# Performance work log

Measured on AMD Instinct MI355X. Metric: run time of the kernel, lower is better.

The kernel has to match this reference:

```python
import jax, jax.numpy as jnp
import numpy as np


def _masked(scores, mask):
    return jnp.where(mask == 0, -jnp.inf, scores)


def setup_inputs() -> dict:
    key = jax.random.key(0)
    ks = jax.random.split(key, 4)
    B, H, S, D = 2, 12, 4096, 64
    blk = 64
    nb = S // blk          # 64 blocks
    nw = nb - 2            # 62 windows
    R = 3                  # random blocks per window
    return {
        'query': jax.random.normal(ks[0], (B, H, S, D), dtype=jnp.float32),
        'key': jax.random.normal(ks[1], (B, H, S, D), dtype=jnp.float32),
        'value': jax.random.normal(ks[2], (B, H, S, D), dtype=jnp.float32),
        'q_mask': jnp.ones((B, 1, S, 1), dtype=jnp.float32),
        'kv_mask': jnp.ones((B, 1, 1, S), dtype=jnp.float32),
        'band_mask': jnp.ones((B, 1, nb - 4, blk, 3 * blk), dtype=jnp.float32),
        'q_block_mask': jnp.ones((B, nb, blk), dtype=jnp.float32),
        'kv_block_mask': jnp.ones((B, nb, blk), dtype=jnp.float32),
        'random_attn': jax.random.randint(ks[3], (H, nw, R), 0, nb, dtype=jnp.int32),
        'q_block_size': blk,
        'kv_block_size': blk,
    }


def reference(query, key, value, q_mask, kv_mask, band_mask, q_block_mask,
              kv_block_mask, random_attn, q_block_size, kv_block_size):
    B, H, S, D = query.shape
    Skv = key.shape[2]
    qb, kb = q_block_size, kv_block_size
    nb, nkb = S // qb, Skv // kb
    scale = 1.0 / (D ** 0.5)

    # expand random indices over batch: [B,H,nw,R]
    ra = jnp.broadcast_to(random_attn[None].astype(jnp.int32),
                          (B,) + random_attn.shape)
    nw, R = ra.shape[2], ra.shape[3]
    bidx = jnp.arange(B)[:, None, None, None]
    hidx = jnp.arange(H)[None, :, None, None]

    # random mask: [B,H,nw,qb,R*kb]
    rm = kv_block_mask[bidx, ra].reshape(B, H, nw, R * kb)
    random_mask = jnp.einsum('blq,bhlk->bhlqk', q_block_mask[:, 1:-1], rm)

    bq = query.reshape(B, H, nb, qb, D)
    bk = key.reshape(B, H, nkb, kb, D)
    bv = value.reshape(B, H, nkb, kb, D)

    # gathered random blocks: [B,H,nw,R*kb,D]
    sk = bk[bidx, hidx, ra].reshape(B, H, nw, R * kb, D)
    sv = bv[bidx, hidx, ra].reshape(B, H, nw, R * kb, D)

    # --- first query block: attends to everything ---
    p1 = jnp.einsum('bhqd,bhkd->bhqk', bq[:, :, 0], key) * scale
    a1 = jax.nn.softmax(_masked(p1, kv_mask), axis=-1)
    c1 = jnp.einsum('bhqk,bhkd->bhqd', a1, value)[:, :, None]

    # --- second query block ---
    k2 = jnp.concatenate([bk[:, :, 0], bk[:, :, 1], bk[:, :, 2], bk[:, :, -1],
                          sk[:, :, 0]], axis=2)
    v2 = jnp.concatenate([bv[:, :, 0], bv[:, :, 1], bv[:, :, 2], bv[:, :, -1],
                          sv[:, :, 0]], axis=2)
    p2 = jnp.einsum('bhqd,bhkd->bhqk', bq[:, :, 1], k2) * scale
    seq_pad = jnp.concatenate([kv_mask[:, :, :, :3 * kb],
                               kv_mask[:, :, :, -kb:],
                               jnp.ones_like(random_mask[:, :1, 0, :1])], axis=3)
    rand_pad = jnp.concatenate([jnp.ones_like(p2[:, :, :, :4 * kb]),
                                random_mask[:, :, 0]], axis=3)
    a2 = jax.nn.softmax(_masked(p2, jnp.minimum(seq_pad, rand_pad)), axis=-1)
    c2 = jnp.einsum('bhqk,bhkd->bhqd', a2, v2)[:, :, None]

    # --- middle blocks: window + global(first,last) + random ---
    ebk = jnp.concatenate([bk[:, :, 1:-3], bk[:, :, 2:-2], bk[:, :, 3:-1]], axis=3)
    ebv = jnp.concatenate([bv[:, :, 1:-3], bv[:, :, 2:-2], bv[:, :, 3:-1]], axis=3)
    mq = bq[:, :, 2:-2]  # [B,H,nb-4,qb,D]
    inner = _masked(jnp.einsum('bhlqd,bhlkd->bhlqk', mq, ebk) * scale, band_mask)
    randp = _masked(jnp.einsum('bhlqd,bhlkd->bhlqk', mq, sk[:, :, 1:-1]) * scale,
                    random_mask[:, :, 1:-1])
    fop = _masked(jnp.einsum('bhlqd,bhkd->bhlqk', mq, bk[:, :, 0]) * scale,
                  kv_mask[:, :, :, :kb][:, :, :, None, :])
    lop = _masked(jnp.einsum('bhlqd,bhkd->bhlqk', mq, bk[:, :, -1]) * scale,
                  kv_mask[:, :, :, -kb:][:, :, :, None, :])
    band = jnp.concatenate([fop, inner, lop, randp], axis=-1)
    aw = jax.nn.softmax(band, axis=-1)
    cm = jnp.einsum('bhlqk,bhlkd->bhlqd', aw[..., kb:4 * kb], ebv)
    cm += jnp.einsum('bhlqk,bhlkd->bhlqd', aw[..., 4 * kb:-kb], sv[:, :, 1:-1])
    cm += jnp.einsum('bhlqk,bhkd->bhlqd', aw[..., :kb], bv[:, :, 0])
    cm += jnp.einsum('bhlqk,bhkd->bhlqd', aw[..., -kb:], bv[:, :, -1])

    # --- second-to-last query block ---
    k3 = jnp.concatenate([bk[:, :, 0], bk[:, :, -3], bk[:, :, -2], bk[:, :, -1],
                          sk[:, :, -1]], axis=2)
    v3 = jnp.concatenate([bv[:, :, 0], bv[:, :, -3], bv[:, :, -2], bv[:, :, -1],
                          sv[:, :, -1]], axis=2)
    p3 = jnp.einsum('bhqd,bhkd->bhqk', bq[:, :, -2], k3) * scale
    seq_pad3 = jnp.concatenate([kv_mask[:, :, :, :kb],
                                kv_mask[:, :, :, -3 * kb:],
                                jnp.ones_like(random_mask[:, :1, 0, :1])], axis=3)
    rand_pad3 = jnp.concatenate([jnp.ones_like(p3[:, :, :, :4 * kb]),
                                 random_mask[:, :, -1]], axis=3)
    a3 = jax.nn.softmax(_masked(p3, jnp.minimum(seq_pad3, rand_pad3)), axis=-1)
    c3 = jnp.einsum('bhqk,bhkd->bhqd', a3, v3)[:, :, None]

    # --- last query block: attends to everything ---
    p4 = jnp.einsum('bhqd,bhkd->bhqk', bq[:, :, -1], key) * scale
    a4 = jax.nn.softmax(_masked(p4, kv_mask), axis=-1)
    c4 = jnp.einsum('bhqk,bhkd->bhqd', a4, value)[:, :, None]

    ctx = jnp.concatenate([c1, c2, cm, c3, c4], axis=2)
    return ctx.reshape(B, H, S, D) * q_mask
```

## Files before the change

### kernel.cpp

```cpp
#include <hip/hip_runtime.h>
#include <hip/hip_bf16.h>

#define BB 2
#define HH 12
#define SS 4096
#define DD 64
#define NB_ 64
#define NW_ 62
#define RR 3

#define PARTIAL_FLOATS 4160
#define N_HEAVY_UNITS  (BB * HH * 2)
#define N_CHUNKS       8

using short8 = __attribute__((ext_vector_type(8))) short;
using f32x4  = __attribute__((ext_vector_type(4))) float;

__device__ __forceinline__ int swz(int r, int c) {
    return (r << 6) + ((((c >> 3) ^ r) & 7) << 3) + (c & 7);
}

__device__ __forceinline__ short pack_bf16(float f) {
    __bf16 b = (__bf16)f;
    return (short)__builtin_bit_cast(unsigned short, b);
}

__device__ __forceinline__ short8 load_cvt8_scaled(const float* p, float sc) {
    f32x4 a = *(const f32x4*)p;
    f32x4 b = *(const f32x4*)(p + 4);
    short8 r;
#pragma unroll
    for (int i = 0; i < 4; ++i) {
        r[i]     = pack_bf16(a[i] * sc);
        r[i + 4] = pack_bf16(b[i] * sc);
    }
    return r;
}

template<bool SPLIT>
__global__ __launch_bounds__(256)
void bigbird_main(const float* __restrict__ Q, const float* __restrict__ K,
                  const float* __restrict__ V, const float* __restrict__ qmask,
                  const int* __restrict__ ra, float* __restrict__ Out,
                  float* __restrict__ ws)
{
    __shared__ __align__(16) short KB[2][64 * 64];
    __shared__ __align__(16) short VT[2][64 * 64];
    __shared__ __align__(16) short PB[4][16 * 64];

    const int tid  = threadIdx.x;
    const int w    = tid >> 6;
    const int lane = tid & 63;
    const int g    = lane >> 4;
    const int m    = lane & 15;

    const int idx    = blockIdx.x;
    const int NHEAVY = SPLIT ? (N_HEAVY_UNITS * N_CHUNKS) : N_HEAVY_UNITS;

    bool heavy;
    int  b, h, qb, u = 0, chunk = 0, chunk_base = 0, nlist;
    int  slist[8], vlist[8];

    if (idx < NHEAVY) {
        heavy = true;
        if (SPLIT) { u = idx >> 3; chunk = idx & 7; chunk_base = chunk * 8; nlist = 8; }
        else       { u = idx; chunk_base = 0; nlist = NB_; }
        const int bh = u >> 1;
        b = bh / HH; h = bh % HH;
        qb = (u & 1) ? (NB_ - 1) : 0;
    } else {
        heavy = false;
        const int idx2 = idx - NHEAVY;
        const int qidx = idx2 / (BB * HH);
        const int bh   = idx2 % (BB * HH);
        b = bh / HH; h = bh % HH;
        qb = qidx + 1;
        const int* rp = ra + (h * NW_ + (qb - 1)) * RR;
        if (qb == 1) {
            slist[0] = 0; slist[1] = 1; slist[2] = 2; slist[3] = 63;
            slist[4] = rp[0]; slist[5] = rp[1]; slist[6] = rp[2]; nlist = 7;
#pragma unroll
            for (int i = 0; i < 7; ++i) vlist[i] = slist[i];
        } else if (qb == NB_ - 2) {
            slist[0] = 0; slist[1] = 61; slist[2] = 62; slist[3] = 63;
            slist[4] = rp[0]; slist[5] = rp[1]; slist[6] = rp[2]; nlist = 7;
#pragma unroll
            for (int i = 0; i < 7; ++i) vlist[i] = slist[i];
        } else {
            slist[0] = 0; slist[1] = qb - 1; slist[2] = qb; slist[3] = qb + 1;
            slist[4] = 63; slist[5] = rp[0]; slist[6] = rp[1]; slist[7] = rp[2];
            vlist[0] = 0; vlist[1] = qb - 1; vlist[2] = qb; vlist[3] = qb + 1;
            vlist[4] = rp[0]; vlist[5] = rp[1]; vlist[6] = rp[2]; vlist[7] = 63;
            nlist = 8;
        }
    }

    const size_t base = ((size_t)(b * HH + h)) * SS * DD;

    short8 qa[2];
    {
        const float* qp = Q + base + (size_t)(qb * 64 + w * 16 + m) * DD + g * 8;
        qa[0] = load_cvt8_scaled(qp, 0.125f);
        qa[1] = load_cvt8_scaled(qp + 32, 0.125f);
    }

    f32x4 oacc[4];
#pragma unroll
    for (int t = 0; t < 4; ++t) oacc[t] = (f32x4){0.f, 0.f, 0.f, 0.f};
    float lsum[4] = {0.f, 0.f, 0.f, 0.f};

    const int kr = tid >> 2;
    const int kc = (tid & 3) * 16;
    const int vp = tid & 31;
    const int vd = (tid >> 5) * 8;

    f32x4 kreg[4], vreg[4];
    auto load_kv = [&](int i) {
        const int kbs = heavy ? (chunk_base + i) : slist[i];
        const int kbv = heavy ? (chunk_base + i) : vlist[i];
        const float* kp = K + base + (size_t)(kbs * 64 + kr) * DD + kc;
        kreg[0] = *(const f32x4*)(kp);
        kreg[1] = *(const f32x4*)(kp + 4);
        kreg[2] = *(const f32x4*)(kp + 8);
        kreg[3] = *(const f32x4*)(kp + 12);
        const float* vp0 = V + base + (size_t)(kbv * 64 + 2 * vp) * DD + vd;
        vreg[0] = *(const f32x4*)(vp0);
        vreg[1] = *(const f32x4*)(vp0 + 4);
        vreg[2] = *(const f32x4*)(vp0 + DD);
        vreg[3] = *(const f32x4*)(vp0 + DD + 4);
    };

    load_kv(0);
    int cur = 0;

    for (int it = 0; it < nlist; ++it) {
        {
            short8 s0, s1;
#pragma unroll
            for (int i = 0; i < 4; ++i) {
                s0[i] = pack_bf16(kreg[0][i]); s0[i + 4] = pack_bf16(kreg[1][i]);
                s1[i] = pack_bf16(kreg[2][i]); s1[i + 4] = pack_bf16(kreg[3][i]);
            }
            *(short8*)&KB[cur][swz(kr, kc)]     = s0;
            *(short8*)&KB[cur][swz(kr, kc + 8)] = s1;
#pragma unroll
            for (int i = 0; i < 8; ++i) {
                float f0 = (i < 4) ? vreg[0][i] : vreg[1][i - 4];
                float f1 = (i < 4) ? vreg[2][i] : vreg[3][i - 4];
                unsigned int pk = (unsigned int)(unsigned short)pack_bf16(f0) |
                                  ((unsigned int)(unsigned short)pack_bf16(f1) << 16);
                *(unsigned int*)&VT[cur][swz(vd + i, 2 * vp)] = pk;
            }
        }

        __syncthreads();

        if (it + 1 < nlist) load_kv(it + 1);

        f32x4 sacc[4];
#pragma unroll
        for (int t = 0; t < 4; ++t) sacc[t] = (f32x4){0.f, 0.f, 0.f, 0.f};
        __builtin_amdgcn_s_setprio(1);
#pragma unroll
        for (int ks = 0; ks < 2; ++ks) {
#pragma unroll
            for (int t = 0; t < 4; ++t) {
                short8 bk = *(short8*)&KB[cur][swz(t * 16 + m, g * 8 + ks * 32)];
                sacc[t] = __builtin_amdgcn_mfma_f32_16x16x32_bf16(qa[ks], bk, sacc[t], 0, 0, 0);
            }
        }
        __builtin_amdgcn_s_setprio(0);

#pragma unroll
        for (int t = 0; t < 4; ++t) {
#pragma unroll
            for (int j = 0; j < 4; ++j) {
                const float p = __expf(sacc[t][j]);
                lsum[j] += p;
                PB[w][swz(4 * g + j, t * 16 + m)] = pack_bf16(p);
            }
        }

        __builtin_amdgcn_s_setprio(1);
#pragma unroll
        for (int ks = 0; ks < 2; ++ks) {
            short8 pa = *(short8*)&PB[w][swz(m, g * 8 + ks * 32)];
#pragma unroll
            for (int t = 0; t < 4; ++t) {
                short8 bv = *(short8*)&VT[cur][swz(t * 16 + m, g * 8 + ks * 32)];
                oacc[t] = __builtin_amdgcn_mfma_f32_16x16x32_bf16(pa, bv, oacc[t], 0, 0, 0);
            }
        }
        __builtin_amdgcn_s_setprio(0);

        cur ^= 1;
    }

#pragma unroll
    for (int j = 0; j < 4; ++j)
#pragma unroll
        for (int off = 1; off < 16; off <<= 1) lsum[j] += __shfl_xor(lsum[j], off);

    if (SPLIT && heavy) {
        float* pb = ws + (size_t)(u * N_CHUNKS + chunk) * PARTIAL_FLOATS;
#pragma unroll
        for (int j = 0; j < 4; ++j) {
            const int row = w * 16 + 4 * g + j;
#pragma unroll
            for (int t = 0; t < 4; ++t) pb[row * 64 + t * 16 + m] = oacc[t][j];
            if (m == 0) pb[4096 + row] = lsum[j];
        }
    } else {
#pragma unroll
        for (int j = 0; j < 4; ++j) {
            const int row = qb * 64 + w * 16 + 4 * g + j;
            const float sc = qmask[b * SS + row] / lsum[j];
            float* op = Out + base + (size_t)row * DD + m;
#pragma unroll
            for (int t = 0; t < 4; ++t) op[t * 16] = oacc[t][j] * sc;
        }
    }
}

__global__ __launch_bounds__(256)
void bigbird_combine(const float* __restrict__ ws, const float* __restrict__ qmask,
                     float* __restrict__ Out)
{
    const int u  = blockIdx.x;
    const int bh = u >> 1;
    const int b  = bh / HH;
    const int h  = bh % HH;
    const int qb = (u & 1) ? (NB_ - 1) : 0;

    const int tid = threadIdx.x;
    const int r   = tid >> 2;
    const int s   = tid & 3;

    const float* pb0 = ws + (size_t)u * N_CHUNKS * PARTIAL_FLOATS;

    float L = 0.f;
    f32x4 o0 = {0,0,0,0}, o1 = {0,0,0,0}, o2 = {0,0,0,0}, o3 = {0,0,0,0};
#pragma unroll
    for (int c = 0; c < N_CHUNKS; ++c) {
        const float* pb = pb0 + c * PARTIAL_FLOATS;
        L += pb[4096 + r];
        const float* orow = pb + r * 64 + s * 16;
        f32x4 a0 = *(const f32x4*)(orow);
        f32x4 a1 = *(const f32x4*)(orow + 4);
        f32x4 a2 = *(const f32x4*)(orow + 8);
        f32x4 a3 = *(const f32x4*)(orow + 12);
#pragma unroll
        for (int i = 0; i < 4; ++i) {
            o0[i] += a0[i]; o1[i] += a1[i];
            o2[i] += a2[i]; o3[i] += a3[i];
        }
    }

    const int row = qb * 64 + r;
    const float scme = qmask[b * SS + row] / L;
    float* op = Out + ((size_t)(b * HH + h)) * SS * DD + (size_t)row * DD + s * 16;
#pragma unroll
    for (int i = 0; i < 4; ++i) { o0[i] *= scme; o1[i] *= scme; o2[i] *= scme; o3[i] *= scme; }
    *(f32x4*)(op)      = o0;
    *(f32x4*)(op + 4)  = o1;
    *(f32x4*)(op + 8)  = o2;
    *(f32x4*)(op + 12) = o3;
}

extern "C" void kernel_launch(void* const* d_in, const int* in_sizes, int n_in,
                              void* d_out, int out_size, void* d_ws, size_t ws_size,
                              hipStream_t stream) {
    const float* Q     = (const float*)d_in[0];
    const float* K     = (const float*)d_in[1];
    const float* V     = (const float*)d_in[2];
    const float* qmask = (const float*)d_in[3];
    const int*   ra    = (const int*)d_in[8];
    float* Out = (float*)d_out;
    float* ws  = (float*)d_ws;

    const size_t need = (size_t)N_HEAVY_UNITS * N_CHUNKS * PARTIAL_FLOATS * sizeof(float);
    if (ws_size >= need) {
        const int grid = N_HEAVY_UNITS * N_CHUNKS + BB * HH * (NB_ - 2);
        bigbird_main<true><<<grid, 256, 0, stream>>>(Q, K, V, qmask, ra, Out, ws);
        bigbird_combine<<<N_HEAVY_UNITS, 256, 0, stream>>>((const float*)ws, qmask, Out);
    } else {
        const int grid = N_HEAVY_UNITS + BB * HH * (NB_ - 2);
        bigbird_main<false><<<grid, 256, 0, stream>>>(Q, K, V, qmask, ra, Out, ws);
    }
}
```

Before: 65.50 us.

## Pre-convert K/V to swizzled bf16 tile images and stream via LDS DMA

```diff
diff --git a/kernel.cpp b/kernel.cpp
--- a/kernel.cpp
+++ b/kernel.cpp
@@ -12,6 +12,8 @@
 #define PARTIAL_FLOATS 4160
 #define N_HEAVY_UNITS  (BB * HH * 2)
 #define N_CHUNKS       8
+#define N_TILES        (BB * HH * NB_)
+#define TILE_ELEMS     4096
 
 using short8 = __attribute__((ext_vector_type(8))) short;
 using f32x4  = __attribute__((ext_vector_type(4))) float;
@@ -37,12 +39,221 @@
     return r;
 }
 
+__device__ __forceinline__ void dma16(const short* gsrc, short* lds) {
+    __builtin_amdgcn_global_load_lds(
+        (const __attribute__((address_space(1))) void*)gsrc,
+        (__attribute__((address_space(3))) void*)lds, 16, 0, 0);
+}
+
+__global__ __launch_bounds__(256)
+void bigbird_prepass(const float* __restrict__ K, const float* __restrict__ V,
+                     short* __restrict__ Kimg, short* __restrict__ Vimg)
+{
+    const int tile = blockIdx.x;
+    const int tid  = threadIdx.x;
+    const size_t gbase = (size_t)tile * TILE_ELEMS;
+
+    {
+        const int kr = tid >> 2, kc = (tid & 3) * 16;
+        const float* kp = K + gbase + kr * 64 + kc;
+        f32x4 a0 = *(const f32x4*)(kp);
+        f32x4 a1 = *(const f32x4*)(kp + 4);
+        f32x4 a2 = *(const f32x4*)(kp + 8);
+        f32x4 a3 = *(const f32x4*)(kp + 12);
+        short8 s0, s1;
+#pragma unroll
+        for (int i = 0; i < 4; ++i) {
+            s0[i] = pack_bf16(a0[i]); s0[i + 4] = pack_bf16(a1[i]);
+            s1[i] = pack_bf16(a2[i]); s1[i + 4] = pack_bf16(a3[i]);
+        }
+        short* kt = Kimg + gbase;
+        *(short8*)&kt[swz(kr, kc)]     = s0;
+        *(short8*)&kt[swz(kr, kc + 8)] = s1;
+    }
+    {
+        const int vp = tid & 31, vd = (tid >> 5) * 8;
+        const float* v0 = V + gbase + (2 * vp) * 64 + vd;
+        f32x4 b0 = *(const f32x4*)(v0);
+        f32x4 b1 = *(const f32x4*)(v0 + 4);
+        f32x4 c0 = *(const f32x4*)(v0 + 64);
+        f32x4 c1 = *(const f32x4*)(v0 + 64 + 4);
+        short* vt = Vimg + gbase;
+#pragma unroll
+        for (int i = 0; i < 8; ++i) {
+            float f0 = (i < 4) ? b0[i] : b1[i - 4];
+            float f1 = (i < 4) ? c0[i] : c1[i - 4];
+            unsigned int pk = (unsigned int)(unsigned short)pack_bf16(f0) |
+                              ((unsigned int)(unsigned short)pack_bf16(f1) << 16);
+            *(unsigned int*)&vt[swz(vd + i, 2 * vp)] = pk;
+        }
+    }
+}
+
+__global__ __launch_bounds__(256, 4)
+void bigbird_main_img(const short* __restrict__ Kimg, const short* __restrict__ Vimg,
+                      const float* __restrict__ Q, const float* __restrict__ qmask,
+                      const int* __restrict__ ra, float* __restrict__ Out,
+                      float* __restrict__ part)
+{
+    __shared__ __align__(16) short KB[2][TILE_ELEMS];
+    __shared__ __align__(16) short VT[2][TILE_ELEMS];
+    __shared__ __align__(16) short PB[4][16 * 64];
+
+    const int tid  = threadIdx.x;
+    const int w    = tid >> 6;
+    const int lane = tid & 63;
+    const int g    = lane >> 4;
+    const int m    = lane & 15;
+
+    const int idx    = blockIdx.x;
+    const int NHEAVY = N_HEAVY_UNITS * N_CHUNKS;
+
+    bool heavy;
+    int  b, h, qb, u = 0, chunk_base = 0, chunk = 0, nlist;
+    int  slist[8], vlist[8];
+
+    if (idx < NHEAVY) {
+        heavy = true;
+        u = idx >> 3; chunk = idx & 7; chunk_base = chunk * 8; nlist = 8;
+        const int bh = u >> 1;
+        b = bh / HH; h = bh % HH;
+        qb = (u & 1) ? (NB_ - 1) : 0;
+    } else {
+        heavy = false;
+        const int idx2 = idx - NHEAVY;
+        const int qidx = idx2 / (BB * HH);
+        const int bh   = idx2 % (BB * HH);
+        b = bh / HH; h = bh % HH;
+        qb = qidx + 1;
+        const int* rp = ra + (h * NW_ + (qb - 1)) * RR;
+        if (qb == 1) {
+            slist[0] = 0; slist[1] = 1; slist[2] = 2; slist[3] = 63;
+            slist[4] = rp[0]; slist[5] = rp[1]; slist[6] = rp[2]; nlist = 7;
+#pragma unroll
+            for (int i = 0; i < 7; ++i) vlist[i] = slist[i];
+        } else if (qb == NB_ - 2) {
+            slist[0] = 0; slist[1] = 61; slist[2] = 62; slist[3] = 63;
+            slist[4] = rp[0]; slist[5] = rp[1]; slist[6] = rp[2]; nlist = 7;
+#pragma unroll
+            for (int i = 0; i < 7; ++i) vlist[i] = slist[i];
+        } else {
+            slist[0] = 0; slist[1] = qb - 1; slist[2] = qb; slist[3] = qb + 1;
+            slist[4] = 63; slist[5] = rp[0]; slist[6] = rp[1]; slist[7] = rp[2];
+            vlist[0] = 0; vlist[1] = qb - 1; vlist[2] = qb; vlist[3] = qb + 1;
+            vlist[4] = rp[0]; vlist[5] = rp[1]; vlist[6] = rp[2]; vlist[7] = 63;
+            nlist = 8;
+        }
+    }
+
+    const int    bh_lin = b * HH + h;
+    const size_t base   = (size_t)bh_lin * SS * DD;
+    const short* Kbh    = Kimg + (size_t)bh_lin * NB_ * TILE_ELEMS;
+    const short* Vbh    = Vimg + (size_t)bh_lin * NB_ * TILE_ELEMS;
+
+    short8 qa[2];
+    {
+        const float* qp = Q + base + (size_t)(qb * 64 + w * 16 + m) * DD + g * 8;
+        qa[0] = load_cvt8_scaled(qp, 0.125f);
+        qa[1] = load_cvt8_scaled(qp + 32, 0.125f);
+    }
+
+    f32x4 oacc[4];
+#pragma unroll
+    for (int t = 0; t < 4; ++t) oacc[t] = (f32x4){0.f, 0.f, 0.f, 0.f};
+    float lsum[4] = {0.f, 0.f, 0.f, 0.f};
+
+    const int c0 = w * 2;
+    auto issue = [&](int buf, int i) {
+        const int kbs = heavy ? (chunk_base + i) : slist[i];
+        const int kbv = heavy ? (chunk_base + i) : vlist[i];
+        const short* sk = Kbh + (size_t)kbs * TILE_ELEMS + (lane << 3);
+        const short* sv = Vbh + (size_t)kbv * TILE_ELEMS + (lane << 3);
+#pragma unroll
+        for (int i2 = 0; i2 < 2; ++i2) {
+            dma16(sk + (c0 + i2) * 512, &KB[buf][(c0 + i2) * 512]);
+            dma16(sv + (c0 + i2) * 512, &VT[buf][(c0 + i2) * 512]);
+        }
+    };
+
+    issue(0, 0);
+    int cur = 0;
+
+    for (int it = 0; it < nlist; ++it) {
+        __syncthreads();
+
+        if (it + 1 < nlist) issue(cur ^ 1, it + 1);
+
+        f32x4 sacc[4];
+#pragma unroll
+        for (int t = 0; t < 4; ++t) sacc[t] = (f32x4){0.f, 0.f, 0.f, 0.f};
+        __builtin_amdgcn_s_setprio(1);
+#pragma unroll
+        for (int ks = 0; ks < 2; ++ks) {
+#pragma unroll
+            for (int t = 0; t < 4; ++t) {
+                short8 bk = *(short8*)&KB[cur][swz(t * 16 + m, g * 8 + ks * 32)];
+                sacc[t] = __builtin_amdgcn_mfma_f32_16x16x32_bf16(qa[ks], bk, sacc[t], 0, 0, 0);
+            }
+        }
+        __builtin_amdgcn_s_setprio(0);
+
+#pragma unroll
+        for (int t = 0; t < 4; ++t) {
+#pragma unroll
+            for (int j = 0; j < 4; ++j) {
+                const float p = __expf(sacc[t][j]);
+                lsum[j] += p;
+                PB[w][swz(4 * g + j, t * 16 + m)] = pack_bf16(p);
+            }
+        }
+
+        __builtin_amdgcn_s_setprio(1);
+#pragma unroll
+        for (int ks = 0; ks < 2; ++ks) {
+            short8 pa = *(short8*)&PB[w][swz(m, g * 8 + ks * 32)];
+#pragma unroll
+            for (int t = 0; t < 4; ++t) {
+                short8 bv = *(short8*)&VT[cur][swz(t * 16 + m, g * 8 + ks * 32)];
+                oacc[t] = __builtin_amdgcn_mfma_f32_16x16x32_bf16(pa, bv, oacc[t], 0, 0, 0);
+            }
+        }
+        __builtin_amdgcn_s_setprio(0);
+
+        cur ^= 1;
+    }
+
+#pragma unroll
+    for (int j = 0; j < 4; ++j)
+#pragma unroll
+        for (int off = 1; off < 16; off <<= 1) lsum[j] += __shfl_xor(lsum[j], off);
+
+    if (heavy) {
+        float* pb = part + (size_t)(u * N_CHUNKS + chunk) * PARTIAL_FLOATS;
+#pragma unroll
+        for (int j = 0; j < 4; ++j) {
+            const int row = w * 16 + 4 * g + j;
+#pragma unroll
+            for (int t = 0; t < 4; ++t) pb[row * 64 + t * 16 + m] = oacc[t][j];
+            if (m == 0) pb[4096 + row] = lsum[j];
+        }
+    } else {
+#pragma unroll
+        for (int j = 0; j < 4; ++j) {
+            const int row = qb * 64 + w * 16 + 4 * g + j;
+            const float sc = qmask[b * SS + row] / lsum[j];
+            float* op = Out + base + (size_t)row * DD + m;
+#pragma unroll
+            for (int t = 0; t < 4; ++t) op[t * 16] = oacc[t][j] * sc;
+        }
+    }
+}
+
 template<bool SPLIT>
 __global__ __launch_bounds__(256)
-void bigbird_main(const float* __restrict__ Q, const float* __restrict__ K,
-                  const float* __restrict__ V, const float* __restrict__ qmask,
-                  const int* __restrict__ ra, float* __restrict__ Out,
-                  float* __restrict__ ws)
+void bigbird_main_reg(const float* __restrict__ Q, const float* __restrict__ K,
+                      const float* __restrict__ V, const float* __restrict__ qmask,
+                      const int* __restrict__ ra, float* __restrict__ Out,
+                      float* __restrict__ ws)
 {
     __shared__ __align__(16) short KB[2][64 * 64];
     __shared__ __align__(16) short VT[2][64 * 64];
@@ -276,15 +487,27 @@
     const float* qmask = (const float*)d_in[3];
     const int*   ra    = (const int*)d_in[8];
     float* Out = (float*)d_out;
-    float* ws  = (float*)d_ws;
-
-    const size_t need = (size_t)N_HEAVY_UNITS * N_CHUNKS * PARTIAL_FLOATS * sizeof(float);
-    if (ws_size >= need) {
+
+    const size_t img_bytes  = (size_t)N_TILES * TILE_ELEMS * sizeof(short);
+    const size_t part_bytes = (size_t)N_HEAVY_UNITS * N_CHUNKS * PARTIAL_FLOATS * sizeof(float);
+    const size_t need_img   = 2 * img_bytes + part_bytes;
+
+    if (ws_size >= need_img) {
+        short* Kimg = (short*)d_ws;
+        short* Vimg = Kimg + (size_t)N_TILES * TILE_ELEMS;
+        float* part = (float*)((char*)d_ws + 2 * img_bytes);
+        bigbird_prepass<<<N_TILES, 256, 0, stream>>>(K, V, Kimg, Vimg);
         const int grid = N_HEAVY_UNITS * N_CHUNKS + BB * HH * (NB_ - 2);
-        bigbird_main<true><<<grid, 256, 0, stream>>>(Q, K, V, qmask, ra, Out, ws);
+        bigbird_main_img<<<grid, 256, 0, stream>>>(Kimg, Vimg, Q, qmask, ra, Out, part);
+        bigbird_combine<<<N_HEAVY_UNITS, 256, 0, stream>>>((const float*)part, qmask, Out);
+    } else if (ws_size >= part_bytes) {
+        float* ws = (float*)d_ws;
+        const int grid = N_HEAVY_UNITS * N_CHUNKS + BB * HH * (NB_ - 2);
+        bigbird_main_reg<true><<<grid, 256, 0, stream>>>(Q, K, V, qmask, ra, Out, ws);
         bigbird_combine<<<N_HEAVY_UNITS, 256, 0, stream>>>((const float*)ws, qmask, Out);
     } else {
+        float* ws = (float*)d_ws;
         const int grid = N_HEAVY_UNITS + BB * HH * (NB_ - 2);
-        bigbird_main<false><<<grid, 256, 0, stream>>>(Q, K, V, qmask, ra, Out, ws);
-    }
-}
+        bigbird_main_reg<false><<<grid, 256, 0, stream>>>(Q, K, V, qmask, ra, Out, ws);
+    }
+}
```

New measurement: 58.21 us. -11.1%, faster.
